# Performance work log

Hardware: AMD Instinct MI355X
Metric: run time of the kernel (lower is better)

Reference implementation:

```python
import jax, jax.numpy as jnp
import numpy as np

N = 50000
E = 800000
NODE_CAT = 20
EDGE_CAT = 4
NODE_CONT = 16
EDGE_CONT = 12
NODE_IN = NODE_CAT + NODE_CONT   # 36
EDGE_IN = EDGE_CAT + EDGE_CONT   # 16
C_HID = 128
C_OUT = 64
HEADS = 2
BN_EPS = 1e-5


def setup_inputs() -> dict:
    key = jax.random.key(0)
    ks = jax.random.split(key, 40)
    g = lambda i, shape, s=0.05: jax.random.normal(ks[i], shape, jnp.float32) * s
    return {
        "x_cat": jax.random.randint(ks[0], (N, 1), 0, NODE_CAT),
        "x_cont": jax.random.normal(ks[1], (N, NODE_CONT), jnp.float32),
        "edge_cat": jax.random.randint(ks[2], (E, 1), 0, EDGE_CAT),
        "edge_cont": jax.random.normal(ks[3], (E, EDGE_CONT), jnp.float32),
        "edge_index": jax.random.randint(ks[4], (2, E), 0, N),
        "node_emb": g(5, (NODE_CAT, NODE_CAT), 1.0),
        "edge_emb": g(6, (EDGE_CAT, EDGE_CAT), 1.0),
        "eps1": jnp.zeros((), jnp.float32),
        "lin_e_W1": g(7, (EDGE_IN, NODE_IN)),
        "lin_e_b1": jnp.zeros((NODE_IN,), jnp.float32),
        "nn_W1": g(8, (NODE_IN, C_HID)),
        "nn_b1": jnp.zeros((C_HID,), jnp.float32),
        "bn_g1": jnp.ones((C_HID,), jnp.float32),
        "bn_b1": jnp.zeros((C_HID,), jnp.float32),
        "bn_m1": g(9, (C_HID,)),
        "bn_v1": jax.random.uniform(ks[10], (C_HID,), jnp.float32) + 0.5,
        "eps2": jnp.zeros((), jnp.float32),
        "lin_e_W2": g(11, (EDGE_IN, C_HID)),
        "lin_e_b2": jnp.zeros((C_HID,), jnp.float32),
        "nn_W2": g(12, (C_HID, C_HID)),
        "nn_b2": jnp.zeros((C_HID,), jnp.float32),
        "bn_g2": jnp.ones((C_HID,), jnp.float32),
        "bn_b2": jnp.zeros((C_HID,), jnp.float32),
        "bn_m2": g(13, (C_HID,)),
        "bn_v2": jax.random.uniform(ks[14], (C_HID,), jnp.float32) + 0.5,
        "Wl": g(15, (C_HID, HEADS * C_OUT)),
        "bl": jnp.zeros((HEADS * C_OUT,), jnp.float32),
        "Wr": g(16, (C_HID, HEADS * C_OUT)),
        "br": jnp.zeros((HEADS * C_OUT,), jnp.float32),
        "We_g": g(17, (EDGE_IN, HEADS * C_OUT)),
        "att": g(18, (HEADS, C_OUT), 0.1),
        "gat_bias": jnp.zeros((C_OUT,), jnp.float32),
    }


def _gine(x, src, dst, ea, eps, WeW, Web, WnW, Wnb):
    # GINEConv: out = nn((1+eps)*x + sum_j relu(x_j + lin_edge(e_ij)))
    msg = jax.nn.relu(x[src] + ea @ WeW + Web)                 # [E, F]
    agg = jax.ops.segment_sum(msg, dst, num_segments=x.shape[0])
    return ((1.0 + eps) * x + agg) @ WnW + Wnb


def _bn(x, g, b, m, v):
    # BatchNorm1d in eval mode with running stats
    return g * (x - m) * jax.lax.rsqrt(v + BN_EPS) + b


def _gatv2(x, src, dst, ea, Wl, bl, Wr, br, We, att, bias):
    n = x.shape[0]
    # PyG GATv2Conv default: add self loops; self-loop edge_attr = mean of edge_attr
    loop = jnp.arange(n)
    src2 = jnp.concatenate([src, loop])
    dst2 = jnp.concatenate([dst, loop])
    ea2 = jnp.concatenate([ea, jnp.broadcast_to(ea.mean(0), (n, ea.shape[1]))], 0)
    xl = (x @ Wl + bl).reshape(n, HEADS, C_OUT)                # source transform
    xr = (x @ Wr + br).reshape(n, HEADS, C_OUT)                # target transform
    ee = (ea2 @ We).reshape(-1, HEADS, C_OUT)
    m = jax.nn.leaky_relu(xl[src2] + xr[dst2] + ee, 0.2)       # [E2, H, C]
    alpha = (m * att).sum(-1)                                  # [E2, H]
    # segment softmax over destination nodes (stable)
    amax = jax.ops.segment_max(alpha, dst2, num_segments=n)
    ex = jnp.exp(alpha - amax[dst2])
    den = jax.ops.segment_sum(ex, dst2, num_segments=n)
    a = ex / den[dst2]
    out = jax.ops.segment_sum(a[:, :, None] * xl[src2], dst2, num_segments=n)
    return out.mean(1) + bias                                  # concat=False -> head mean


def reference(x_cat, x_cont, edge_cat, edge_cont, edge_index, node_emb, edge_emb,
              eps1, lin_e_W1, lin_e_b1, nn_W1, nn_b1, bn_g1, bn_b1, bn_m1, bn_v1,
              eps2, lin_e_W2, lin_e_b2, nn_W2, nn_b2, bn_g2, bn_b2, bn_m2, bn_v2,
              Wl, bl, Wr, br, We_g, att, gat_bias):
    src, dst = edge_index[0], edge_index[1]
    x = jnp.concatenate([node_emb[x_cat[:, 0]], x_cont], -1)       # [N, 36]
    ea = jnp.concatenate([edge_emb[edge_cat[:, 0]], edge_cont], -1)  # [E, 16]
    h = _gine(x, src, dst, ea, eps1, lin_e_W1, lin_e_b1, nn_W1, nn_b1)
    h = _bn(jax.nn.relu(h), bn_g1, bn_b1, bn_m1, bn_v1)            # dropout = identity (eval)
    h = _gine(h, src, dst, ea, eps2, lin_e_W2, lin_e_b2, nn_W2, nn_b2)
    h = _bn(jax.nn.relu(h), bn_g2, bn_b2, bn_m2, bn_v2)
    return _gatv2(h, src, dst, ea, Wl, bl, Wr, br, We_g, att, gat_bias)
```

## Files before the change

### kernel.cpp

```cpp
#include <hip/hip_runtime.h>
#include <math.h>

#define N_NODES 50000
#define N_EDGES 800000
#define NODE_IN 36
#define EDGE_IN 16
#define C_HID 128
#define C_OUT 64
#define BN_EPS 1e-5f
#define DT_NT 32

#define SB_T 512
#define SB_N ((N_NODES + SB_T - 1) / SB_T)

#define NF_BLOCKS ((N_NODES * NODE_IN + 255) / 256)
#define DEG_BLOCKS ((N_EDGES + 255) / 256)
#define EAS_BLOCKS 512

typedef __attribute__((ext_vector_type(2))) float v2f;

__device__ __forceinline__ int rfl(int v) { return __builtin_amdgcn_readfirstlane(v); }

__device__ __forceinline__ v2f v2(float s) { v2f r; r.x = s; r.y = s; return r; }

__device__ __forceinline__ v2f unpack_bf2(unsigned u) {
    v2f r;
    r.x = __uint_as_float(u << 16);
    r.y = __uint_as_float(u & 0xFFFF0000u);
    return r;
}
__device__ __forceinline__ unsigned pack_bf2(float lo, float hi) {
    unsigned ul = __float_as_uint(lo); ul += 0x7FFF + ((ul >> 16) & 1);
    unsigned uh = __float_as_uint(hi); uh += 0x7FFF + ((uh >> 16) & 1);
    return (ul >> 16) | (uh & 0xFFFF0000u);
}

__device__ __forceinline__ v2f sel4v(int cat, v2f a, v2f b, v2f c, v2f d) {
    v2f r = (cat == 0) ? a : b;
    r = (cat == 2) ? c : r;
    r = (cat == 3) ? d : r;
    return r;
}
__device__ __forceinline__ float sel4(int cat, float a, float b, float c, float d) {
    float r = (cat == 0) ? a : b;
    r = (cat == 2) ? c : r;
    r = (cat == 3) ? d : r;
    return r;
}

__device__ __forceinline__ float merge_pair(float x, float y, int off) {
    bool hi = (threadIdx.x & off) != 0;
    float send = hi ? x : y;
    float recv = __shfl_xor(send, off);
    return (hi ? y : x) + recv;
}

__global__ void k_prep(const int* __restrict__ xcat,
                       const float* __restrict__ xcont,
                       const float* __restrict__ node_emb,
                       const int* __restrict__ ei,
                       const int* __restrict__ ecat,
                       const float* __restrict__ econt,
                       float* __restrict__ x,
                       int* __restrict__ deg,
                       float* __restrict__ ea_sum) {
    int bb = blockIdx.x;
    if (bb < NF_BLOCKS) {
        int idx = bb * 256 + threadIdx.x;
        if (idx >= N_NODES * NODE_IN) return;
        int i = idx / NODE_IN;
        int j = idx - i * NODE_IN;
        float v;
        if (j < 20) v = node_emb[xcat[i] * 20 + j];
        else        v = xcont[i * 16 + (j - 20)];
        x[idx] = v;
        return;
    }
    if (bb < NF_BLOCKS + DEG_BLOCKS) {
        int e = (bb - NF_BLOCKS) * 256 + threadIdx.x;
        if (e >= N_EDGES) return;
        atomicAdd(deg + ei[N_EDGES + e], 1);
        return;
    }
    int blk = bb - NF_BLOCKS - DEG_BLOCKS;
    float p[12];
#pragma unroll
    for (int k = 0; k < 12; k++) p[k] = 0.f;
    float cnt[4] = {0.f, 0.f, 0.f, 0.f};
    const int stride = EAS_BLOCKS * 256;
    for (int e = blk * 256 + threadIdx.x; e < N_EDGES; e += stride) {
        int c = ecat[e];
        cnt[0] += (c == 0) ? 1.f : 0.f;
        cnt[1] += (c == 1) ? 1.f : 0.f;
        cnt[2] += (c == 2) ? 1.f : 0.f;
        cnt[3] += (c == 3) ? 1.f : 0.f;
        const float4* v4 = (const float4*)(econt + (size_t)e * 12);
        float4 a = v4[0], bq = v4[1], d = v4[2];
        p[0] += a.x;  p[1] += a.y;  p[2] += a.z;  p[3] += a.w;
        p[4] += bq.x; p[5] += bq.y; p[6] += bq.z; p[7] += bq.w;
        p[8] += d.x;  p[9] += d.y;  p[10] += d.z; p[11] += d.w;
    }
    float vals[16];
#pragma unroll
    for (int k = 0; k < 12; k++) vals[k] = p[k];
#pragma unroll
    for (int k = 0; k < 4; k++) vals[12 + k] = cnt[k];
#pragma unroll
    for (int k = 0; k < 16; k++) {
        float v = vals[k];
#pragma unroll
        for (int off = 32; off > 0; off >>= 1) v += __shfl_xor(v, off);
        vals[k] = v;
    }
    __shared__ float red[4][16];
    int wid = threadIdx.x >> 6, lane = threadIdx.x & 63;
    if (lane == 0) {
#pragma unroll
        for (int k = 0; k < 16; k++) red[wid][k] = vals[k];
    }
    __syncthreads();
    if (threadIdx.x < 16) {
        float s = red[0][threadIdx.x] + red[1][threadIdx.x] +
                  red[2][threadIdx.x] + red[3][threadIdx.x];
        atomicAdd(ea_sum + threadIdx.x, s);
    }
}

__global__ void k_scan1(const int* __restrict__ deg, int* __restrict__ bsum) {
    int i = blockIdx.x * SB_T + threadIdx.x;
    int v = (i < N_NODES) ? deg[i] : 0;
#pragma unroll
    for (int off = 32; off > 0; off >>= 1) v += __shfl_xor(v, off);
    __shared__ int red[SB_T / 64];
    int wid = threadIdx.x >> 6, lane = threadIdx.x & 63;
    if (lane == 0) red[wid] = v;
    __syncthreads();
    if (threadIdx.x == 0) {
        int s = 0;
#pragma unroll
        for (int w = 0; w < SB_T / 64; w++) s += red[w];
        bsum[blockIdx.x] = s;
    }
}

__global__ void k_scan2(const int* __restrict__ bsum, int* __restrict__ boff,
                        int* __restrict__ rowp) {
    __shared__ int s[128];
    int t = threadIdx.x;
    int v = (t < SB_N) ? bsum[t] : 0;
    s[t] = v;
    __syncthreads();
    for (int off = 1; off < 128; off <<= 1) {
        int u = (t >= off) ? s[t - off] : 0;
        __syncthreads();
        s[t] += u;
        __syncthreads();
    }
    if (t < SB_N) boff[t] = s[t] - v;
    if (t == SB_N - 1) rowp[N_NODES] = s[t];
}

__global__ void k_scan3(const int* __restrict__ deg, const int* __restrict__ boff,
                        int* __restrict__ rowp, int* __restrict__ cursor) {
    int b = blockIdx.x, t = threadIdx.x;
    int i = b * SB_T + t;
    int d = (i < N_NODES) ? deg[i] : 0;
    int lane = t & 63;
    int v = d;
#pragma unroll
    for (int off = 1; off < 64; off <<= 1) {
        int u = __shfl_up(v, off);
        if (lane >= off) v += u;
    }
    __shared__ int wsum[SB_T / 64];
    int wid = t >> 6;
    if (lane == 63) wsum[wid] = v;
    __syncthreads();
    int wo = 0;
    for (int w = 0; w < wid; w++) wo += wsum[w];
    int excl = boff[b] + wo + v - d;
    if (i < N_NODES) { rowp[i] = excl; cursor[i] = excl; }
}

__global__ void k_fill(const int* __restrict__ ei, const int* __restrict__ ecat,
                       const float* __restrict__ econt,
                       int* __restrict__ cursor, int* __restrict__ csr_ps,
                       float* __restrict__ csr_e) {
    int e = blockIdx.x * blockDim.x + threadIdx.x;
    if (e >= N_EDGES) return;
    int d = ei[N_EDGES + e];
    const float4* s4 = (const float4*)(econt + (size_t)e * 12);
    float4 a = s4[0], b = s4[1], c = s4[2];
    int pos = atomicAdd(cursor + d, 1);
    csr_ps[pos] = ei[e] | (ecat[e] << 24);
    float4* d4 = (float4*)(csr_e + (size_t)pos * 12);
    d4[0] = a; d4[1] = b; d4[2] = c;
}

__global__ void k_gine1_gather(const int* __restrict__ rowp,
                               const int* __restrict__ csr_ps,
                               const float* __restrict__ csr_e,
                               const float* __restrict__ edge_emb,
                               const float* __restrict__ W,
                               const float* __restrict__ b,
                               const float* __restrict__ x,
                               float* __restrict__ agg) {
    int i = blockIdx.x * 4 + (threadIdx.x >> 6);
    int lane = threadIdx.x & 63;
    if (i >= N_NODES) return;
    int c = (lane < NODE_IN) ? lane : (NODE_IN - 1);
    float w[12];
#pragma unroll
    for (int k = 0; k < 12; k++) w[k] = W[(4 + k) * NODE_IN + c];
    float tb[4];
#pragma unroll
    for (int q = 0; q < 4; q++) {
        float v = b[c];
#pragma unroll
        for (int k = 0; k < 4; k++) v += edge_emb[q * 4 + k] * W[k * NODE_IN + c];
        tb[q] = v;
    }
    int beg = rfl(rowp[i]), end = rfl(rowp[i + 1]);
    float acc = 0.f;
    int p = beg;
    for (; p + 4 <= end; p += 4) {
        int ps4[4];
        float4 A[4], B[4], C4[4];
        float xs[4];
#pragma unroll
        for (int bq = 0; bq < 4; bq++) {
            const float4* ec4 = (const float4*)(csr_e + (size_t)(p + bq) * 12);
            A[bq] = ec4[0]; B[bq] = ec4[1]; C4[bq] = ec4[2];
            ps4[bq] = rfl(csr_ps[p + bq]);
            xs[bq] = x[(size_t)(ps4[bq] & 0xFFFFFF) * NODE_IN + c];
        }
#pragma unroll
        for (int bq = 0; bq < 4; bq++) {
            int cat = ps4[bq] >> 24;
            float t = sel4(cat, tb[0], tb[1], tb[2], tb[3]);
            t += A[bq].x * w[0] + A[bq].y * w[1] + A[bq].z * w[2] + A[bq].w * w[3];
            t += B[bq].x * w[4] + B[bq].y * w[5] + B[bq].z * w[6] + B[bq].w * w[7];
            t += C4[bq].x * w[8] + C4[bq].y * w[9] + C4[bq].z * w[10] + C4[bq].w * w[11];
            acc += fmaxf(xs[bq] + t, 0.f);
        }
    }
    for (; p < end; ++p) {
        int ps = rfl(csr_ps[p]);
        int src = ps & 0xFFFFFF, cat = ps >> 24;
        const float4* ec4 = (const float4*)(csr_e + (size_t)p * 12);
        float4 A = ec4[0], B = ec4[1], C4 = ec4[2];
        float t = sel4(cat, tb[0], tb[1], tb[2], tb[3]);
        t += A.x * w[0] + A.y * w[1] + A.z * w[2] + A.w * w[3];
        t += B.x * w[4] + B.y * w[5] + B.z * w[6] + B.w * w[7];
        t += C4.x * w[8] + C4.y * w[9] + C4.z * w[10] + C4.w * w[11];
        acc += fmaxf(x[(size_t)src * NODE_IN + c] + t, 0.f);
    }
    if (lane < NODE_IN) agg[(size_t)i * NODE_IN + lane] = acc;
}

__global__ __launch_bounds__(256, 4) void k_gine1_node(
        const float* __restrict__ x, const float* __restrict__ agg,
        const float* __restrict__ eps_p,
        const float* __restrict__ W,
        const float* __restrict__ b, const float* __restrict__ g,
        const float* __restrict__ bb, const float* __restrict__ m,
        const float* __restrict__ v, unsigned* __restrict__ h1p) {
    __shared__ float sW[NODE_IN * C_HID];
    __shared__ float sz[DT_NT * NODE_IN];
    int tid = threadIdx.x;
    int node0 = blockIdx.x * DT_NT;
    float eps = eps_p[0];
    {
        const float4* Wv = (const float4*)W;
        float4* sWv = (float4*)sW;
        for (int t = tid; t < NODE_IN * C_HID / 4; t += 256) sWv[t] = Wv[t];
    }
    {
        int nmax = min(DT_NT, N_NODES - node0);
        int tot = nmax * NODE_IN / 4;
        const float4* xv = (const float4*)(x + (size_t)node0 * NODE_IN);
        const float4* av = (const float4*)(agg + (size_t)node0 * NODE_IN);
        float4* szv = (float4*)sz;
        float s = 1.f + eps;
        for (int t = tid; t < tot; t += 256) {
            float4 a = xv[t], c = av[t];
            float4 r;
            r.x = s * a.x + c.x; r.y = s * a.y + c.y;
            r.z = s * a.z + c.z; r.w = s * a.w + c.w;
            szv[t] = r;
        }
    }
    __syncthreads();
    int cg = tid & 15, c0 = cg * 4;
    int n0 = (tid >> 4) * 2;
    float4 bL = *(const float4*)&b[c0];
    float4 bH = *(const float4*)&b[c0 + 64];
    float accL[2][4], accH[2][4];
#pragma unroll
    for (int n = 0; n < 2; n++) {
        accL[n][0] = bL.x; accL[n][1] = bL.y; accL[n][2] = bL.z; accL[n][3] = bL.w;
        accH[n][0] = bH.x; accH[n][1] = bH.y; accH[n][2] = bH.z; accH[n][3] = bH.w;
    }
#pragma unroll 2
    for (int jb = 0; jb < NODE_IN; jb += 4) {
#pragma unroll
        for (int r = 0; r < 4; r++) {
            float4 wl = *(const float4*)&sW[(jb + r) * C_HID + c0];
            float4 wh = *(const float4*)&sW[(jb + r) * C_HID + c0 + 64];
#pragma unroll
            for (int n = 0; n < 2; n++) {
                float zz = sz[(n0 + n) * NODE_IN + jb + r];
                accL[n][0] += zz * wl.x; accL[n][1] += zz * wl.y;
                accL[n][2] += zz * wl.z; accL[n][3] += zz * wl.w;
                accH[n][0] += zz * wh.x; accH[n][1] += zz * wh.y;
                accH[n][2] += zz * wh.z; accH[n][3] += zz * wh.w;
            }
        }
    }
    float4 gL = *(const float4*)&g[c0],  gH = *(const float4*)&g[c0 + 64];
    float4 mL = *(const float4*)&m[c0],  mH = *(const float4*)&m[c0 + 64];
    float4 vL = *(const float4*)&v[c0],  vH = *(const float4*)&v[c0 + 64];
    float4 bbL = *(const float4*)&bb[c0], bbH = *(const float4*)&bb[c0 + 64];
    float scL[4] = { gL.x * rsqrtf(vL.x + BN_EPS), gL.y * rsqrtf(vL.y + BN_EPS),
                     gL.z * rsqrtf(vL.z + BN_EPS), gL.w * rsqrtf(vL.w + BN_EPS) };
    float scH[4] = { gH.x * rsqrtf(vH.x + BN_EPS), gH.y * rsqrtf(vH.y + BN_EPS),
                     gH.z * rsqrtf(vH.z + BN_EPS), gH.w * rsqrtf(vH.w + BN_EPS) };
    float mLa[4] = { mL.x, mL.y, mL.z, mL.w }, mHa[4] = { mH.x, mH.y, mH.z, mH.w };
    float bbLa[4] = { bbL.x, bbL.y, bbL.z, bbL.w }, bbHa[4] = { bbH.x, bbH.y, bbH.z, bbH.w };
#pragma unroll
    for (int n = 0; n < 2; n++) {
        int i = node0 + n0 + n;
        if (i < N_NODES) {
            uint4 o;
            unsigned* po = (unsigned*)&o;
#pragma unroll
            for (int k = 0; k < 4; k++) {
                float lo = (fmaxf(accL[n][k], 0.f) - mLa[k]) * scL[k] + bbLa[k];
                float hi = (fmaxf(accH[n][k], 0.f) - mHa[k]) * scH[k] + bbHa[k];
                po[k] = pack_bf2(lo, hi);
            }
            *(uint4*)&h1p[(size_t)i * 64 + c0] = o;
        }
    }
}

__global__ void k_gine2_gather(const int* __restrict__ rowp,
                               const int* __restrict__ csr_ps,
                               const float* __restrict__ csr_e,
                               const float* __restrict__ edge_emb,
                               const float* __restrict__ W,
                               const float* __restrict__ b,
                               const unsigned* __restrict__ h1p,
                               float2* __restrict__ aggp) {
    int i = blockIdx.x * 4 + (threadIdx.x >> 6);
    int lane = threadIdx.x & 63;
    if (i >= N_NODES) return;
    v2f w01[12];
#pragma unroll
    for (int k = 0; k < 12; k++) {
        w01[k].x = W[(4 + k) * C_HID + lane];
        w01[k].y = W[(4 + k) * C_HID + lane + 64];
    }
    v2f tb01[4];
#pragma unroll
    for (int q = 0; q < 4; q++) {
        v2f t; t.x = b[lane]; t.y = b[lane + 64];
#pragma unroll
        for (int k = 0; k < 4; k++) {
            float ev = edge_emb[q * 4 + k];
            t.x += ev * W[k * C_HID + lane];
            t.y += ev * W[k * C_HID + lane + 64];
        }
        tb01[q] = t;
    }
    const v2f zero = v2(0.f);
    int beg = rfl(rowp[i]), end = rfl(rowp[i + 1]);
    v2f acc01 = zero;
    int p = beg;
    for (; p + 4 <= end; p += 4) {
        int ps4[4];
        float4 A[4], B[4], C4[4];
        v2f xs[4];
#pragma unroll
        for (int bq = 0; bq < 4; bq++) {
            const float4* ec4 = (const float4*)(csr_e + (size_t)(p + bq) * 12);
            A[bq] = ec4[0]; B[bq] = ec4[1]; C4[bq] = ec4[2];
            ps4[bq] = rfl(csr_ps[p + bq]);
            xs[bq] = unpack_bf2(h1p[(size_t)(ps4[bq] & 0xFFFFFF) * 64 + lane]);
        }
#pragma unroll
        for (int bq = 0; bq < 4; bq++) {
            int cat = ps4[bq] >> 24;
            v2f t = sel4v(cat, tb01[0], tb01[1], tb01[2], tb01[3]);
            t = __builtin_elementwise_fma(v2(A[bq].x), w01[0], t);
            t = __builtin_elementwise_fma(v2(A[bq].y), w01[1], t);
            t = __builtin_elementwise_fma(v2(A[bq].z), w01[2], t);
            t = __builtin_elementwise_fma(v2(A[bq].w), w01[3], t);
            t = __builtin_elementwise_fma(v2(B[bq].x), w01[4], t);
            t = __builtin_elementwise_fma(v2(B[bq].y), w01[5], t);
            t = __builtin_elementwise_fma(v2(B[bq].z), w01[6], t);
            t = __builtin_elementwise_fma(v2(B[bq].w), w01[7], t);
            t = __builtin_elementwise_fma(v2(C4[bq].x), w01[8], t);
            t = __builtin_elementwise_fma(v2(C4[bq].y), w01[9], t);
            t = __builtin_elementwise_fma(v2(C4[bq].z), w01[10], t);
            t = __builtin_elementwise_fma(v2(C4[bq].w), w01[11], t);
            acc01 += __builtin_elementwise_max(xs[bq] + t, zero);
        }
    }
    for (; p < end; ++p) {
        int ps = rfl(csr_ps[p]);
        int src = ps & 0xFFFFFF, cat = ps >> 24;
        const float4* ec4 = (const float4*)(csr_e + (size_t)p * 12);
        float4 A = ec4[0], B = ec4[1], C4 = ec4[2];
        v2f xs = unpack_bf2(h1p[(size_t)src * 64 + lane]);
        v2f t = sel4v(cat, tb01[0], tb01[1], tb01[2], tb01[3]);
        t = __builtin_elementwise_fma(v2(A.x), w01[0], t);
        t = __builtin_elementwise_fma(v2(A.y), w01[1], t);
        t = __builtin_elementwise_fma(v2(A.z), w01[2], t);
        t = __builtin_elementwise_fma(v2(A.w), w01[3], t);
        t = __builtin_elementwise_fma(v2(B.x), w01[4], t);
        t = __builtin_elementwise_fma(v2(B.y), w01[5], t);
        t = __builtin_elementwise_fma(v2(B.z), w01[6], t);
        t = __builtin_elementwise_fma(v2(B.w), w01[7], t);
        t = __builtin_elementwise_fma(v2(C4.x), w01[8], t);
        t = __builtin_elementwise_fma(v2(C4.y), w01[9], t);
        t = __builtin_elementwise_fma(v2(C4.z), w01[10], t);
        t = __builtin_elementwise_fma(v2(C4.w), w01[11], t);
        acc01 += __builtin_elementwise_max(xs + t, zero);
    }
    float2 o; o.x = acc01.x; o.y = acc01.y;
    aggp[(size_t)i * 64 + lane] = o;
}

__global__ __launch_bounds__(256, 3) void k_gine2_gat0(
        const unsigned* __restrict__ h1p, const float2* __restrict__ aggp,
        const float* __restrict__ eps_p,
        const float* __restrict__ W,
        const float* __restrict__ b, const float* __restrict__ g,
        const float* __restrict__ bb, const float* __restrict__ m,
        const float* __restrict__ v,
        const float* __restrict__ Wl, const float* __restrict__ bl,
        const float* __restrict__ Wr, const float* __restrict__ br,
        const float* __restrict__ ea_sum, const float* __restrict__ edge_emb,
        const float* __restrict__ We,
        unsigned* __restrict__ xlp, float2* __restrict__ xrp,
        float* __restrict__ ee_loop) {
    __shared__ float sW[64 * C_HID];
    __shared__ float sz[DT_NT * C_HID];
    int tid = threadIdx.x;
    int node0 = blockIdx.x * DT_NT;
    float eps = eps_p[0];
    if (blockIdx.x == 0 && tid < C_HID) {
        const float inv = 1.f / (float)N_EDGES;
        float acc = 0.f;
#pragma unroll
        for (int k = 0; k < 4; k++) {
            float s = 0.f;
#pragma unroll
            for (int q = 0; q < 4; q++) s += ea_sum[12 + q] * edge_emb[q * 4 + k];
            acc += (s * inv) * We[k * C_HID + tid];
        }
#pragma unroll
        for (int k = 0; k < 12; k++)
            acc += (ea_sum[k] * inv) * We[(4 + k) * C_HID + tid];
        ee_loop[tid] = acc;
    }
    {
        int nmax = min(DT_NT, N_NODES - node0);
        int tot = nmax * 64;
        float s = 1.f + eps;
        for (int t = tid; t < tot; t += 256) {
            int n = t >> 6, pp = t & 63;
            v2f h = unpack_bf2(h1p[(size_t)(node0 + n) * 64 + pp]);
            float2 a = aggp[(size_t)(node0 + n) * 64 + pp];
            sz[n * C_HID + pp]      = s * h.x + a.x;
            sz[n * C_HID + pp + 64] = s * h.y + a.y;
        }
    }
    int cg2 = tid & 31, c02 = cg2 * 4;
    int n02 = (tid >> 5) * 4;
    float4 bi = *(const float4*)&b[c02];
    float acc[4][4];
#pragma unroll
    for (int n = 0; n < 4; n++) {
        acc[n][0] = bi.x; acc[n][1] = bi.y; acc[n][2] = bi.z; acc[n][3] = bi.w;
    }
    for (int half = 0; half < 2; half++) {
        __syncthreads();
        {
            const float4* Wv = (const float4*)(W + half * 64 * C_HID);
            float4* sWv = (float4*)sW;
            for (int t = tid; t < 64 * C_HID / 4; t += 256) sWv[t] = Wv[t];
        }
        __syncthreads();
        int jbase = half * 64;
#pragma unroll 2
        for (int jb = 0; jb < 64; jb += 4) {
            float4 w0 = *(const float4*)&sW[(jb + 0) * C_HID + c02];
            float4 w1 = *(const float4*)&sW[(jb + 1) * C_HID + c02];
            float4 w2 = *(const float4*)&sW[(jb + 2) * C_HID + c02];
            float4 w3 = *(const float4*)&sW[(jb + 3) * C_HID + c02];
#pragma unroll
            for (int n = 0; n < 4; n++) {
                float4 zz = *(const float4*)&sz[(n02 + n) * C_HID + jbase + jb];
                acc[n][0] += zz.x * w0.x + zz.y * w1.x + zz.z * w2.x + zz.w * w3.x;
                acc[n][1] += zz.x * w0.y + zz.y * w1.y + zz.z * w2.y + zz.w * w3.y;
                acc[n][2] += zz.x * w0.z + zz.y * w1.z + zz.z * w2.z + zz.w * w3.z;
                acc[n][3] += zz.x * w0.w + zz.y * w1.w + zz.z * w2.w + zz.w * w3.w;
            }
        }
    }
    {
        float4 gg = *(const float4*)&g[c02];
        float4 mm = *(const float4*)&m[c02];
        float4 vv = *(const float4*)&v[c02];
        float4 bbv = *(const float4*)&bb[c02];
        float4 sc;
        sc.x = gg.x * rsqrtf(vv.x + BN_EPS); sc.y = gg.y * rsqrtf(vv.y + BN_EPS);
        sc.z = gg.z * rsqrtf(vv.z + BN_EPS); sc.w = gg.w * rsqrtf(vv.w + BN_EPS);
        __syncthreads();
#pragma unroll
        for (int n = 0; n < 4; n++) {
            float* dst = &sz[(n02 + n) * C_HID + c02];
            dst[0] = (fmaxf(acc[n][0], 0.f) - mm.x) * sc.x + bbv.x;
            dst[1] = (fmaxf(acc[n][1], 0.f) - mm.y) * sc.y + bbv.y;
            dst[2] = (fmaxf(acc[n][2], 0.f) - mm.z) * sc.z + bbv.z;
            dst[3] = (fmaxf(acc[n][3], 0.f) - mm.w) * sc.w + bbv.w;
        }
    }
    int cg = tid & 15, c0 = cg * 4;
    int n0 = (tid >> 4) * 2;
    for (int wsel = 0; wsel < 2; wsel++) {
        const float* Wm = wsel ? Wr : Wl;
        const float* bm = wsel ? br : bl;
        float4 bL = *(const float4*)&bm[c0];
        float4 bH = *(const float4*)&bm[c0 + 64];
        float accL[2][4], accH[2][4];
#pragma unroll
        for (int n = 0; n < 2; n++) {
            accL[n][0] = bL.x; accL[n][1] = bL.y; accL[n][2] = bL.z; accL[n][3] = bL.w;
            accH[n][0] = bH.x; accH[n][1] = bH.y; accH[n][2] = bH.z; accH[n][3] = bH.w;
        }
        for (int half = 0; half < 2; half++) {
            __syncthreads();
            {
                const float4* Wv = (const float4*)(Wm + half * 64 * C_HID);
                float4* sWv = (float4*)sW;
                for (int t = tid; t < 64 * C_HID / 4; t += 256) sWv[t] = Wv[t];
            }
            __syncthreads();
            int jbase = half * 64;
#pragma unroll 2
            for (int jb = 0; jb < 64; jb += 4) {
#pragma unroll
                for (int r = 0; r < 4; r++) {
                    float4 wl = *(const float4*)&sW[(jb + r) * C_HID + c0];
                    float4 wh = *(const float4*)&sW[(jb + r) * C_HID + c0 + 64];
#pragma unroll
                    for (int n = 0; n < 2; n++) {
                        float zz = sz[(n0 + n) * C_HID + jbase + jb + r];
                        accL[n][0] += zz * wl.x; accL[n][1] += zz * wl.y;
                        accL[n][2] += zz * wl.z; accL[n][3] += zz * wl.w;
                        accH[n][0] += zz * wh.x; accH[n][1] += zz * wh.y;
                        accH[n][2] += zz * wh.z; accH[n][3] += zz * wh.w;
                    }
                }
            }
        }
#pragma unroll
        for (int n = 0; n < 2; n++) {
            int i = node0 + n0 + n;
            if (i < N_NODES) {
                if (wsel == 0) {
                    uint4 o;
                    unsigned* po = (unsigned*)&o;
#pragma unroll
                    for (int k = 0; k < 4; k++) po[k] = pack_bf2(accL[n][k], accH[n][k]);
                    *(uint4*)&xlp[(size_t)i * 64 + c0] = o;
                } else {
                    float4 o1, o2;
                    o1.x = accL[n][0]; o1.y = accH[n][0]; o1.z = accL[n][1]; o1.w = accH[n][1];
                    o2.x = accL[n][2]; o2.y = accH[n][2]; o2.z = accL[n][3]; o2.w = accH[n][3];
                    *(float4*)&xrp[(size_t)i * 64 + c0] = o1;
                    *(float4*)&xrp[(size_t)i * 64 + c0 + 2] = o2;
                }
            }
        }
    }
}

__global__ void k_gat_fused(const int* __restrict__ rowp,
                            const int* __restrict__ csr_ps,
                            const float* __restrict__ csr_e,
                            const float* __restrict__ edge_emb,
                            const float* __restrict__ We,
                            const float* __restrict__ att,
                            const float* __restrict__ ee_loop,
                            const unsigned* __restrict__ xlp,
                            const float2* __restrict__ xrp,
                            const float* __restrict__ bias,
                            float* __restrict__ out) {
    int i = blockIdx.x * 4 + (threadIdx.x >> 6);
    int lane = threadIdx.x & 63;
    if (i >= N_NODES) return;
    v2f w01[12];
#pragma unroll
    for (int k = 0; k < 12; k++) {
        w01[k].x = We[(4 + k) * C_HID + lane];
        w01[k].y = We[(4 + k) * C_HID + lane + 64];
    }
    v2f tb01[4];
#pragma unroll
    for (int q = 0; q < 4; q++) {
        v2f t = v2(0.f);
#pragma unroll
        for (int k = 0; k < 4; k++) {
            float ev = edge_emb[q * 4 + k];
            t.x += ev * We[k * C_HID + lane];
            t.y += ev * We[k * C_HID + lane + 64];
        }
        tb01[q] = t;
    }
    v2f at01; at01.x = att[lane]; at01.y = att[lane + 64];
    v2f lp01; lp01.x = ee_loop[lane]; lp01.y = ee_loop[lane + 64];
    const v2f zero = v2(0.f);
    const v2f fifth = v2(0.2f);

    float2 xr2 = xrp[(size_t)i * 64 + lane];
    v2f xr01; xr01.x = xr2.x; xr01.y = xr2.y;
    v2f xld01 = unpack_bf2(xlp[(size_t)i * 64 + lane]);

    v2f z01 = xld01 + xr01 + lp01;
    z01 = __builtin_elementwise_max(z01, zero) +
          fifth * __builtin_elementwise_min(z01, zero);
    v2f d01 = z01 * at01;
    {
        float mq = merge_pair(d01.x, d01.y, 1);
        mq += __shfl_xor(mq, 2);
        mq += __shfl_xor(mq, 4);
        mq += __shfl_xor(mq, 8);
        mq += __shfl_xor(mq, 16);
        mq += __shfl_xor(mq, 32);
        int emqi = __float_as_int(__expf(mq));
        d01.x = __int_as_float(__builtin_amdgcn_readlane(emqi, 0));
        d01.y = __int_as_float(__builtin_amdgcn_readlane(emqi, 1));
    }
    v2f den01 = d01;
    v2f acc01 = xld01 * den01;

    int beg = rfl(rowp[i]), end = rfl(rowp[i + 1]);
    int p = beg;
    for (; p + 4 <= end; p += 4) {
        int ps4[4];
        float4 A[4], B[4], C4[4];
        v2f xs[4];
#pragma unroll
        for (int bq = 0; bq < 4; bq++) {
            const float4* ec4 = (const float4*)(csr_e + (size_t)(p + bq) * 12);
            A[bq] = ec4[0]; B[bq] = ec4[1]; C4[bq] = ec4[2];
            ps4[bq] = rfl(csr_ps[p + bq]);
            xs[bq] = unpack_bf2(xlp[(size_t)(ps4[bq] & 0xFFFFFF) * 64 + lane]);
        }
        v2f dd[4];
#pragma unroll
        for (int bq = 0; bq < 4; bq++) {
            int cat = ps4[bq] >> 24;
            v2f e = sel4v(cat, tb01[0], tb01[1], tb01[2], tb01[3]);
            e = __builtin_elementwise_fma(v2(A[bq].x), w01[0], e);
            e = __builtin_elementwise_fma(v2(A[bq].y), w01[1], e);
            e = __builtin_elementwise_fma(v2(A[bq].z), w01[2], e);
            e = __builtin_elementwise_fma(v2(A[bq].w), w01[3], e);
            e = __builtin_elementwise_fma(v2(B[bq].x), w01[4], e);
            e = __builtin_elementwise_fma(v2(B[bq].y), w01[5], e);
            e = __builtin_elementwise_fma(v2(B[bq].z), w01[6], e);
            e = __builtin_elementwise_fma(v2(B[bq].w), w01[7], e);
            e = __builtin_elementwise_fma(v2(C4[bq].x), w01[8], e);
            e = __builtin_elementwise_fma(v2(C4[bq].y), w01[9], e);
            e = __builtin_elementwise_fma(v2(C4[bq].z), w01[10], e);
            e = __builtin_elementwise_fma(v2(C4[bq].w), w01[11], e);
            v2f z = xs[bq] + xr01 + e;
            z = __builtin_elementwise_max(z, zero) +
                fifth * __builtin_elementwise_min(z, zero);
            dd[bq] = z * at01;
        }
        float m01 = merge_pair(dd[0].x, dd[0].y, 1);
        float m23 = merge_pair(dd[1].x, dd[1].y, 1);
        float m45 = merge_pair(dd[2].x, dd[2].y, 1);
        float m67 = merge_pair(dd[3].x, dd[3].y, 1);
        float n0 = merge_pair(m01, m23, 2);
        float n1 = merge_pair(m45, m67, 2);
        float q = merge_pair(n0, n1, 4);
        q += __shfl_xor(q, 8);
        q += __shfl_xor(q, 16);
        q += __shfl_xor(q, 32);
        int eqi = __float_as_int(__expf(q));
        v2f p0, p1, p2, p3;
        p0.x = __int_as_float(__builtin_amdgcn_readlane(eqi, 0));
        p0.y = __int_as_float(__builtin_amdgcn_readlane(eqi, 1));
        p1.x = __int_as_float(__builtin_amdgcn_readlane(eqi, 2));
        p1.y = __int_as_float(__builtin_amdgcn_readlane(eqi, 3));
        p2.x = __int_as_float(__builtin_amdgcn_readlane(eqi, 4));
        p2.y = __int_as_float(__builtin_amdgcn_readlane(eqi, 5));
        p3.x = __int_as_float(__builtin_amdgcn_readlane(eqi, 6));
        p3.y = __int_as_float(__builtin_amdgcn_readlane(eqi, 7));
        den01 += (p0 + p1) + (p2 + p3);
        acc01 = __builtin_elementwise_fma(p0, xs[0], acc01);
        acc01 = __builtin_elementwise_fma(p1, xs[1], acc01);
        acc01 = __builtin_elementwise_fma(p2, xs[2], acc01);
        acc01 = __builtin_elementwise_fma(p3, xs[3], acc01);
    }
    for (; p < end; ++p) {
        int ps = rfl(csr_ps[p]);
        int src = ps & 0xFFFFFF, cat = ps >> 24;
        const float4* ec4 = (const float4*)(csr_e + (size_t)p * 12);
        float4 A = ec4[0], B = ec4[1], C4 = ec4[2];
        v2f xs = unpack_bf2(xlp[(size_t)src * 64 + lane]);
        v2f e = sel4v(cat, tb01[0], tb01[1], tb01[2], tb01[3]);
        e = __builtin_elementwise_fma(v2(A.x), w01[0], e);
        e = __builtin_elementwise_fma(v2(A.y), w01[1], e);
        e = __builtin_elementwise_fma(v2(A.z), w01[2], e);
        e = __builtin_elementwise_fma(v2(A.w), w01[3], e);
        e = __builtin_elementwise_fma(v2(B.x), w01[4], e);
        e = __builtin_elementwise_fma(v2(B.y), w01[5], e);
        e = __builtin_elementwise_fma(v2(B.z), w01[6], e);
        e = __builtin_elementwise_fma(v2(B.w), w01[7], e);
        e = __builtin_elementwise_fma(v2(C4.x), w01[8], e);
        e = __builtin_elementwise_fma(v2(C4.y), w01[9], e);
        e = __builtin_elementwise_fma(v2(C4.z), w01[10], e);
        e = __builtin_elementwise_fma(v2(C4.w), w01[11], e);
        v2f z = xs + xr01 + e;
        z = __builtin_elementwise_max(z, zero) +
            fifth * __builtin_elementwise_min(z, zero);
        v2f a = z * at01;
        float mq = merge_pair(a.x, a.y, 1);
        mq += __shfl_xor(mq, 2);
        mq += __shfl_xor(mq, 4);
        mq += __shfl_xor(mq, 8);
        mq += __shfl_xor(mq, 16);
        mq += __shfl_xor(mq, 32);
        int emqi = __float_as_int(__expf(mq));
        v2f pe;
        pe.x = __int_as_float(__builtin_amdgcn_readlane(emqi, 0));
        pe.y = __int_as_float(__builtin_amdgcn_readlane(emqi, 1));
        den01 += pe;
        acc01 = __builtin_elementwise_fma(pe, xs, acc01);
    }
    out[(size_t)i * C_OUT + lane] =
        0.5f * (acc01.x / den01.x + acc01.y / den01.y) + bias[lane];
}

extern "C" void kernel_launch(void* const* d_in, const int* in_sizes, int n_in,
                              void* d_out, int out_size, void* d_ws, size_t ws_size,
                              hipStream_t stream) {
    const int*   x_cat    = (const int*)d_in[0];
    const float* x_cont   = (const float*)d_in[1];
    const int*   e_cat    = (const int*)d_in[2];
    const float* e_cont   = (const float*)d_in[3];
    const int*   ei       = (const int*)d_in[4];
    const float* node_emb = (const float*)d_in[5];
    const float* edge_emb = (const float*)d_in[6];
    const float* eps1     = (const float*)d_in[7];
    const float* W1e      = (const float*)d_in[8];
    const float* b1e      = (const float*)d_in[9];
    const float* W1n      = (const float*)d_in[10];
    const float* b1n      = (const float*)d_in[11];
    const float* g1       = (const float*)d_in[12];
    const float* bb1      = (const float*)d_in[13];
    const float* m1       = (const float*)d_in[14];
    const float* v1       = (const float*)d_in[15];
    const float* eps2     = (const float*)d_in[16];
    const float* W2e      = (const float*)d_in[17];
    const float* b2e      = (const float*)d_in[18];
    const float* W2n      = (const float*)d_in[19];
    const float* b2n      = (const float*)d_in[20];
    const float* g2       = (const float*)d_in[21];
    const float* bb2      = (const float*)d_in[22];
    const float* m2       = (const float*)d_in[23];
    const float* v2p      = (const float*)d_in[24];
    const float* Wl       = (const float*)d_in[25];
    const float* bl       = (const float*)d_in[26];
    const float* Wr       = (const float*)d_in[27];
    const float* br       = (const float*)d_in[28];
    const float* Weg      = (const float*)d_in[29];
    const float* att      = (const float*)d_in[30];
    const float* gbias    = (const float*)d_in[31];

    const size_t NF128 = (size_t)N_NODES * C_HID;

    float* A = (float*)d_ws;
    float* B = A + NF128;
    unsigned* Hb = (unsigned*)(B + NF128);
    float* ea_sum  = (float*)(Hb + (size_t)N_NODES * 64);
    float* ee_loop = ea_sum + 16;
    float* csr_e = ee_loop + C_HID;
    int* csr_ps  = (int*)(csr_e + (size_t)N_EDGES * 12);
    int* deg     = csr_ps + N_EDGES;
    int* cursor  = deg + N_NODES;
    int* rowp    = cursor + N_NODES;
    int* bsum    = rowp + N_NODES + 1;
    int* boff    = bsum + SB_N;

    float* x = A;
    float* agg36 = B;
    float2* aggp = (float2*)B;
    float2* xrp  = (float2*)B;
    unsigned* h1p = Hb; unsigned* xlp = Hb;

    size_t need = (size_t)((char*)(boff + SB_N) - (char*)d_ws);
    if (ws_size < need) return;

    hipMemsetAsync(deg, 0, N_NODES * sizeof(int), stream);
    hipMemsetAsync(ea_sum, 0, 16 * sizeof(float), stream);

    const int EB = (N_EDGES + 255) / 256;
    const int NB4 = (N_NODES + 3) / 4;
    const int NBD = (N_NODES + DT_NT - 1) / DT_NT;

    k_prep<<<NF_BLOCKS + DEG_BLOCKS + EAS_BLOCKS, 256, 0, stream>>>(
        x_cat, x_cont, node_emb, ei, e_cat, e_cont, x, deg, ea_sum);
    k_scan1<<<SB_N, SB_T, 0, stream>>>(deg, bsum);
    k_scan2<<<1, 128, 0, stream>>>(bsum, boff, rowp);
    k_scan3<<<SB_N, SB_T, 0, stream>>>(deg, boff, rowp, cursor);
    k_fill<<<EB, 256, 0, stream>>>(ei, e_cat, e_cont, cursor, csr_ps, csr_e);

    k_gine1_gather<<<NB4, 256, 0, stream>>>(
        rowp, csr_ps, csr_e, edge_emb, W1e, b1e, x, agg36);
    k_gine1_node<<<NBD, 256, 0, stream>>>(
        x, agg36, eps1, W1n, b1n, g1, bb1, m1, v1, h1p);
    k_gine2_gather<<<NB4, 256, 0, stream>>>(
        rowp, csr_ps, csr_e, edge_emb, W2e, b2e, h1p, aggp);

    k_gine2_gat0<<<NBD, 256, 0, stream>>>(
        h1p, aggp, eps2, W2n, b2n, g2, bb2, m2, v2p,
        Wl, bl, Wr, br, ea_sum, edge_emb, Weg, xlp, xrp, ee_loop);

    k_gat_fused<<<NB4, 256, 0, stream>>>(
        rowp, csr_ps, csr_e, edge_emb, Weg, att, ee_loop,
        xlp, xrp, gbias, (float*)d_out);
}
```

Measured before the change: 540.5 us.

## Use bf16 MFMA for GINE2 node MLP and GAT projections

```diff
diff --git a/kernel.cpp b/kernel.cpp
--- a/kernel.cpp
+++ b/kernel.cpp
@@ -9,6 +9,7 @@
 #define C_OUT 64
 #define BN_EPS 1e-5f
 #define DT_NT 32
+#define ZSTR 136
 
 #define SB_T 512
 #define SB_N ((N_NODES + SB_T - 1) / SB_T)
@@ -18,6 +19,8 @@
 #define EAS_BLOCKS 512
 
 typedef __attribute__((ext_vector_type(2))) float v2f;
+typedef __attribute__((ext_vector_type(8))) short s8v;
+typedef __attribute__((ext_vector_type(4))) float f4v;
 
 __device__ __forceinline__ int rfl(int v) { return __builtin_amdgcn_readfirstlane(v); }
 
@@ -33,6 +36,10 @@
     unsigned ul = __float_as_uint(lo); ul += 0x7FFF + ((ul >> 16) & 1);
     unsigned uh = __float_as_uint(hi); uh += 0x7FFF + ((uh >> 16) & 1);
     return (ul >> 16) | (uh & 0xFFFF0000u);
+}
+__device__ __forceinline__ ushort bf16r(float x) {
+    unsigned u = __float_as_uint(x); u += 0x7FFF + ((u >> 16) & 1);
+    return (ushort)(u >> 16);
 }
 
 __device__ __forceinline__ v2f sel4v(int cat, v2f a, v2f b, v2f c, v2f d) {
@@ -126,6 +133,17 @@
     }
 }
 
+__global__ void k_wconv(const float* __restrict__ W2n, const float* __restrict__ Wl,
+                        const float* __restrict__ Wr, ushort* __restrict__ wtb) {
+    int idx = blockIdx.x * 256 + threadIdx.x;
+    if (idx >= 3 * C_HID * C_HID) return;
+    int mm = idx >> 14;
+    int r = idx & 16383;
+    int n = r >> 7, k = r & 127;
+    const float* src = (mm == 0) ? W2n : (mm == 1 ? Wl : Wr);
+    wtb[idx] = bf16r(src[k * C_HID + n]);
+}
+
 __global__ void k_scan1(const int* __restrict__ deg, int* __restrict__ bsum) {
     int i = blockIdx.x * SB_T + threadIdx.x;
     int v = (i < N_NODES) ? deg[i] : 0;
@@ -432,24 +450,22 @@
     aggp[(size_t)i * 64 + lane] = o;
 }
 
-__global__ __launch_bounds__(256, 3) void k_gine2_gat0(
+__global__ __launch_bounds__(256, 4) void k_gine2_gat0(
         const unsigned* __restrict__ h1p, const float2* __restrict__ aggp,
         const float* __restrict__ eps_p,
-        const float* __restrict__ W,
+        const ushort* __restrict__ wtb,
         const float* __restrict__ b, const float* __restrict__ g,
-        const float* __restrict__ bb, const float* __restrict__ m,
-        const float* __restrict__ v,
-        const float* __restrict__ Wl, const float* __restrict__ bl,
-        const float* __restrict__ Wr, const float* __restrict__ br,
+        const float* __restrict__ bb, const float* __restrict__ bnm,
+        const float* __restrict__ bnv,
+        const float* __restrict__ bl, const float* __restrict__ br,
         const float* __restrict__ ea_sum, const float* __restrict__ edge_emb,
         const float* __restrict__ We,
         unsigned* __restrict__ xlp, float2* __restrict__ xrp,
         float* __restrict__ ee_loop) {
-    __shared__ float sW[64 * C_HID];
-    __shared__ float sz[DT_NT * C_HID];
+    __shared__ ushort zb[DT_NT * ZSTR];
+    __shared__ ushort hb[DT_NT * ZSTR];
     int tid = threadIdx.x;
     int node0 = blockIdx.x * DT_NT;
-    float eps = eps_p[0];
     if (blockIdx.x == 0 && tid < C_HID) {
         const float inv = 1.f / (float)N_EDGES;
         float acc = 0.f;
@@ -467,122 +483,91 @@
     }
     {
         int nmax = min(DT_NT, N_NODES - node0);
-        int tot = nmax * 64;
-        float s = 1.f + eps;
-        for (int t = tid; t < tot; t += 256) {
+        float s = 1.f + eps_p[0];
+        for (int t = tid; t < nmax * 64; t += 256) {
             int n = t >> 6, pp = t & 63;
             v2f h = unpack_bf2(h1p[(size_t)(node0 + n) * 64 + pp]);
             float2 a = aggp[(size_t)(node0 + n) * 64 + pp];
-            sz[n * C_HID + pp]      = s * h.x + a.x;
-            sz[n * C_HID + pp + 64] = s * h.y + a.y;
-        }
-    }
-    int cg2 = tid & 31, c02 = cg2 * 4;
-    int n02 = (tid >> 5) * 4;
-    float4 bi = *(const float4*)&b[c02];
-    float acc[4][4];
-#pragma unroll
-    for (int n = 0; n < 4; n++) {
-        acc[n][0] = bi.x; acc[n][1] = bi.y; acc[n][2] = bi.z; acc[n][3] = bi.w;
-    }
-    for (int half = 0; half < 2; half++) {
-        __syncthreads();
-        {
-            const float4* Wv = (const float4*)(W + half * 64 * C_HID);
-            float4* sWv = (float4*)sW;
-            for (int t = tid; t < 64 * C_HID / 4; t += 256) sWv[t] = Wv[t];
-        }
-        __syncthreads();
-        int jbase = half * 64;
-#pragma unroll 2
-        for (int jb = 0; jb < 64; jb += 4) {
-            float4 w0 = *(const float4*)&sW[(jb + 0) * C_HID + c02];
-            float4 w1 = *(const float4*)&sW[(jb + 1) * C_HID + c02];
-            float4 w2 = *(const float4*)&sW[(jb + 2) * C_HID + c02];
-            float4 w3 = *(const float4*)&sW[(jb + 3) * C_HID + c02];
-#pragma unroll
-            for (int n = 0; n < 4; n++) {
-                float4 zz = *(const float4*)&sz[(n02 + n) * C_HID + jbase + jb];
-                acc[n][0] += zz.x * w0.x + zz.y * w1.x + zz.z * w2.x + zz.w * w3.x;
-                acc[n][1] += zz.x * w0.y + zz.y * w1.y + zz.z * w2.y + zz.w * w3.y;
-                acc[n][2] += zz.x * w0.z + zz.y * w1.z + zz.z * w2.z + zz.w * w3.z;
-                acc[n][3] += zz.x * w0.w + zz.y * w1.w + zz.z * w2.w + zz.w * w3.w;
+            unsigned pk = pack_bf2(s * h.x + a.x, s * h.y + a.y);
+            zb[n * ZSTR + pp]      = (ushort)(pk & 0xFFFFu);
+            zb[n * ZSTR + pp + 64] = (ushort)(pk >> 16);
+        }
+    }
+    __syncthreads();
+    int lane = tid & 63;
+    int w = tid >> 6;
+    int lo4 = lane & 15, hi4 = lane >> 4;
+    int mt = w & 1;
+    {
+        int ntbase = (w >> 1) * 4;
+        const ushort* zrow = &zb[(mt * 16 + lo4) * ZSTR + hi4 * 8];
+        s8v afr[4];
+#pragma unroll
+        for (int ks = 0; ks < 4; ks++) afr[ks] = *(const s8v*)(zrow + ks * 32);
+#pragma unroll
+        for (int j = 0; j < 4; j++) {
+            int nt = ntbase + j;
+            int n = nt * 16 + lo4;
+            const ushort* wrow = wtb + (size_t)n * 128 + hi4 * 8;
+            f4v acc = {0.f, 0.f, 0.f, 0.f};
+#pragma unroll
+            for (int ks = 0; ks < 4; ks++) {
+                s8v bfr = *(const s8v*)(wrow + ks * 32);
+                acc = __builtin_amdgcn_mfma_f32_16x16x32_bf16(afr[ks], bfr, acc, 0, 0, 0);
             }
-        }
-    }
+            float bnb = b[n];
+            float sc = g[n] * rsqrtf(bnv[n] + BN_EPS);
+            float mu = bnm[n], be = bb[n];
+#pragma unroll
+            for (int r = 0; r < 4; r++) {
+                int mrow = mt * 16 + hi4 * 4 + r;
+                float h2v = (fmaxf(acc[r] + bnb, 0.f) - mu) * sc + be;
+                hb[mrow * ZSTR + n] = bf16r(h2v);
+            }
+        }
+    }
+    __syncthreads();
     {
-        float4 gg = *(const float4*)&g[c02];
-        float4 mm = *(const float4*)&m[c02];
-        float4 vv = *(const float4*)&v[c02];
-        float4 bbv = *(const float4*)&bb[c02];
-        float4 sc;
-        sc.x = gg.x * rsqrtf(vv.x + BN_EPS); sc.y = gg.y * rsqrtf(vv.y + BN_EPS);
-        sc.z = gg.z * rsqrtf(vv.z + BN_EPS); sc.w = gg.w * rsqrtf(vv.w + BN_EPS);
-        __syncthreads();
-#pragma unroll
-        for (int n = 0; n < 4; n++) {
-            float* dst = &sz[(n02 + n) * C_HID + c02];
-            dst[0] = (fmaxf(acc[n][0], 0.f) - mm.x) * sc.x + bbv.x;
-            dst[1] = (fmaxf(acc[n][1], 0.f) - mm.y) * sc.y + bbv.y;
-            dst[2] = (fmaxf(acc[n][2], 0.f) - mm.z) * sc.z + bbv.z;
-            dst[3] = (fmaxf(acc[n][3], 0.f) - mm.w) * sc.w + bbv.w;
-        }
-    }
-    int cg = tid & 15, c0 = cg * 4;
-    int n0 = (tid >> 4) * 2;
-    for (int wsel = 0; wsel < 2; wsel++) {
-        const float* Wm = wsel ? Wr : Wl;
-        const float* bm = wsel ? br : bl;
-        float4 bL = *(const float4*)&bm[c0];
-        float4 bH = *(const float4*)&bm[c0 + 64];
-        float accL[2][4], accH[2][4];
-#pragma unroll
-        for (int n = 0; n < 2; n++) {
-            accL[n][0] = bL.x; accL[n][1] = bL.y; accL[n][2] = bL.z; accL[n][3] = bL.w;
-            accH[n][0] = bH.x; accH[n][1] = bH.y; accH[n][2] = bH.z; accH[n][3] = bH.w;
-        }
-        for (int half = 0; half < 2; half++) {
-            __syncthreads();
-            {
-                const float4* Wv = (const float4*)(Wm + half * 64 * C_HID);
-                float4* sWv = (float4*)sW;
-                for (int t = tid; t < 64 * C_HID / 4; t += 256) sWv[t] = Wv[t];
+        int pg = w >> 1;
+        const ushort* hrow = &hb[(mt * 16 + lo4) * ZSTR + hi4 * 8];
+        s8v afr[4];
+#pragma unroll
+        for (int ks = 0; ks < 4; ks++) afr[ks] = *(const s8v*)(hrow + ks * 32);
+        for (int wsel = 0; wsel < 2; wsel++) {
+            const ushort* wt = wtb + (size_t)(1 + wsel) * C_HID * C_HID;
+            const float* bm = wsel ? br : bl;
+            f4v accA[2], accB[2];
+#pragma unroll
+            for (int j = 0; j < 2; j++) {
+                int cA = (pg * 2 + j) * 16 + lo4;
+                const ushort* wrA = wt + (size_t)cA * 128 + hi4 * 8;
+                const ushort* wrB = wt + (size_t)(cA + 64) * 128 + hi4 * 8;
+                f4v aA = {0.f, 0.f, 0.f, 0.f}, aB = {0.f, 0.f, 0.f, 0.f};
+#pragma unroll
+                for (int ks = 0; ks < 4; ks++) {
+                    s8v bA = *(const s8v*)(wrA + ks * 32);
+                    s8v bB = *(const s8v*)(wrB + ks * 32);
+                    aA = __builtin_amdgcn_mfma_f32_16x16x32_bf16(afr[ks], bA, aA, 0, 0, 0);
+                    aB = __builtin_amdgcn_mfma_f32_16x16x32_bf16(afr[ks], bB, aB, 0, 0, 0);
+                }
+                accA[j] = aA; accB[j] = aB;
             }
-            __syncthreads();
-            int jbase = half * 64;
-#pragma unroll 2
-            for (int jb = 0; jb < 64; jb += 4) {
+#pragma unroll
+            for (int j = 0; j < 2; j++) {
+                int c = (pg * 2 + j) * 16 + lo4;
+                float blo = bm[c], bhi = bm[c + 64];
 #pragma unroll
                 for (int r = 0; r < 4; r++) {
-                    float4 wl = *(const float4*)&sW[(jb + r) * C_HID + c0];
-                    float4 wh = *(const float4*)&sW[(jb + r) * C_HID + c0 + 64];
-#pragma unroll
-                    for (int n = 0; n < 2; n++) {
-                        float zz = sz[(n0 + n) * C_HID + jbase + jb + r];
-                        accL[n][0] += zz * wl.x; accL[n][1] += zz * wl.y;
-                        accL[n][2] += zz * wl.z; accL[n][3] += zz * wl.w;
-                        accH[n][0] += zz * wh.x; accH[n][1] += zz * wh.y;
-                        accH[n][2] += zz * wh.z; accH[n][3] += zz * wh.w;
+                    int i = node0 + mt * 16 + hi4 * 4 + r;
+                    if (i < N_NODES) {
+                        float lo = accA[j][r] + blo, hi = accB[j][r] + bhi;
+                        if (wsel == 0) {
+                            xlp[(size_t)i * 64 + c] = pack_bf2(lo, hi);
+                        } else {
+                            float2 o; o.x = lo; o.y = hi;
+                            xrp[(size_t)i * 64 + c] = o;
+                        }
                     }
-                }
-            }
-        }
-#pragma unroll
-        for (int n = 0; n < 2; n++) {
-            int i = node0 + n0 + n;
-            if (i < N_NODES) {
-                if (wsel == 0) {
-                    uint4 o;
-                    unsigned* po = (unsigned*)&o;
-#pragma unroll
-                    for (int k = 0; k < 4; k++) po[k] = pack_bf2(accL[n][k], accH[n][k]);
-                    *(uint4*)&xlp[(size_t)i * 64 + c0] = o;
-                } else {
-                    float4 o1, o2;
-                    o1.x = accL[n][0]; o1.y = accH[n][0]; o1.z = accL[n][1]; o1.w = accH[n][1];
-                    o2.x = accL[n][2]; o2.y = accH[n][2]; o2.z = accL[n][3]; o2.w = accH[n][3];
-                    *(float4*)&xrp[(size_t)i * 64 + c0] = o1;
-                    *(float4*)&xrp[(size_t)i * 64 + c0 + 2] = o2;
                 }
             }
         }
@@ -792,7 +777,8 @@
     unsigned* Hb = (unsigned*)(B + NF128);
     float* ea_sum  = (float*)(Hb + (size_t)N_NODES * 64);
     float* ee_loop = ea_sum + 16;
-    float* csr_e = ee_loop + C_HID;
+    ushort* wtb  = (ushort*)(ee_loop + C_HID);
+    float* csr_e = (float*)(wtb + 3 * C_HID * C_HID);
     int* csr_ps  = (int*)(csr_e + (size_t)N_EDGES * 12);
     int* deg     = csr_ps + N_EDGES;
     int* cursor  = deg + N_NODES;
@@ -815,7 +801,9 @@
     const int EB = (N_EDGES + 255) / 256;
     const int NB4 = (N_NODES + 3) / 4;
     const int NBD = (N_NODES + DT_NT - 1) / DT_NT;
-
+    const int WB = (3 * C_HID * C_HID + 255) / 256;
+
+    k_wconv<<<WB, 256, 0, stream>>>(W2n, Wl, Wr, wtb);
     k_prep<<<NF_BLOCKS + DEG_BLOCKS + EAS_BLOCKS, 256, 0, stream>>>(
         x_cat, x_cont, node_emb, ei, e_cat, e_cont, x, deg, ea_sum);
     k_scan1<<<SB_N, SB_T, 0, stream>>>(deg, bsum);
@@ -831,8 +819,8 @@
         rowp, csr_ps, csr_e, edge_emb, W2e, b2e, h1p, aggp);
 
     k_gine2_gat0<<<NBD, 256, 0, stream>>>(
-        h1p, aggp, eps2, W2n, b2n, g2, bb2, m2, v2p,
-        Wl, bl, Wr, br, ea_sum, edge_emb, Weg, xlp, xrp, ee_loop);
+        h1p, aggp, eps2, wtb, b2n, g2, bb2, m2, v2p,
+        bl, br, ea_sum, edge_emb, Weg, xlp, xrp, ee_loop);
 
     k_gat_fused<<<NB4, 256, 0, stream>>>(
         rowp, csr_ps, csr_e, edge_emb, Weg, att, ee_loop,
```

New measurement: 492.7 us. 8.8% less time.
